# Kernel optimization log

Measured on AMD Instinct MI355X. Metric: run time of the kernel, lower is better.

The kernel has to match this reference:

```python
import jax, jax.numpy as jnp
import numpy as np
from jax import lax

SEQ_LEN = 1024
INPUT_DIM = 64
NUM_HIDDEN = 512
NUM_CLASSES = 10
BATCH = 256
SIGMA = 0.01


def setup_inputs() -> dict:
    key = jax.random.key(0)
    k_x, k_whx, k_whh, k_wph = jax.random.split(key, 4)
    x = jax.random.normal(k_x, (BATCH, SEQ_LEN, INPUT_DIM), dtype=jnp.float32)
    Whx = SIGMA * jax.random.normal(k_whx, (INPUT_DIM, NUM_HIDDEN), dtype=jnp.float32)
    Whh = SIGMA * jax.random.normal(k_whh, (NUM_HIDDEN, NUM_HIDDEN), dtype=jnp.float32)
    Wph = SIGMA * jax.random.normal(k_wph, (NUM_HIDDEN, NUM_CLASSES), dtype=jnp.float32)
    bh = jnp.zeros((NUM_HIDDEN, 1), dtype=jnp.float32)
    bp = jnp.zeros((NUM_CLASSES, 1), dtype=jnp.float32)
    return {"x": x, "Whx": Whx, "Whh": Whh, "Wph": Wph, "bh": bh, "bp": bp}


def reference(x, Whx, Whh, Wph, bh, bp):
    # x: [B, S, D]; h: [B, H]
    B = x.shape[0]
    H = Whh.shape[0]
    bh_row = bh[:, 0]  # per-hidden-unit bias (intended semantics of bh)
    bp_row = bp[:, 0]

    def step(h, xt):
        h_new = jnp.tanh(xt @ Whx + h @ Whh + bh_row)
        return h_new, None

    h0 = jnp.zeros((B, H), dtype=x.dtype)
    xs = jnp.swapaxes(x, 0, 1)  # [S, B, D] for scan over time
    h_final, _ = lax.scan(step, h0, xs)
    p = h_final @ Wph + bp_row  # [B, C]
    return p
```

## Files before the change

### kernel.cpp

```cpp
#include <hip/hip_runtime.h>
#include <hip/hip_bf16.h>
#include <hip/hip_fp8.h>
#include <cstdint>
#include <cstddef>


#define T_SEQ   1024
#define D_IN    64
#define H_DIM   512
#define NB      16
#define NBLK    16
#define NTW     4
#define KS_F16  10
#define KS_REG8 4
#define KS_LDS8 2
#define HSPLIT  320
#define APITCH  848
#define FP8OFF  640
#define ABUF_BYTES (2 * NB * APITCH)
#define WWAVE_BYTES (KS_LDS8 * 2 * 1024)
#define WLDS_BYTES (8 * WWAVE_BYTES)
#define SMEM_TOTAL (ABUF_BYTES + WLDS_BYTES)
#define WSCALE  256.0f
#define HSCALE  128.0f
#define UNSCALE (1.0f / 32768.0f)
#define U_BYTES ((size_t)256 * 1024 * 512 * 2)
#define TT      8
#define NCHUNK  (T_SEQ / TT)
#define NPROD   (NBLK * NCHUNK)
#define FLAG_BYTES (NBLK * NCHUNK * 4)

typedef __attribute__((ext_vector_type(8))) short  short8;
typedef __attribute__((ext_vector_type(4))) short  short4v;
typedef __attribute__((ext_vector_type(4))) float  f32x4;
typedef __attribute__((ext_vector_type(4))) unsigned int uint4v;
typedef __attribute__((ext_vector_type(2))) unsigned int uint2v;

static __device__ __forceinline__ short f16b(float v) {
  return __builtin_bit_cast(short, (_Float16)v);
}
static __device__ __forceinline__ short bf16b(float v) {
  return __builtin_bit_cast(short, __float2bfloat16(v));
}
static __device__ __forceinline__ float f16f(unsigned short u) {
  return (float)__builtin_bit_cast(_Float16, (short)u);
}
static __device__ __forceinline__ unsigned int pk2h(float a, float b) {
#if defined(__has_builtin) && __has_builtin(__builtin_amdgcn_cvt_pkrtz)
  return __builtin_bit_cast(unsigned int, __builtin_amdgcn_cvt_pkrtz(a, b));
#else
  return (unsigned int)(unsigned short)f16b(a) |
         ((unsigned int)(unsigned short)f16b(b) << 16);
#endif
}
static __device__ __forceinline__ float fast_tanh(float x) {
  x = fminf(20.f, fmaxf(-20.f, x));
  const float t = __builtin_amdgcn_exp2f(x * 2.885390081777927f);
  return (t - 1.f) * __builtin_amdgcn_rcpf(t + 1.f);
}
static __device__ __forceinline__ unsigned char f32_to_fp8(float v) {
#if defined(__has_builtin) && __has_builtin(__builtin_amdgcn_cvt_pk_fp8_f32)
  const int r = __builtin_amdgcn_cvt_pk_fp8_f32(v, v, 0, false);
  return (unsigned char)(r & 0xff);
#else
  __hip_fp8_e4m3 f(v);
  return (unsigned char)f.__x;
#endif
}
static __device__ __forceinline__ unsigned int pk4fp8(float a, float b, float c, float d) {
#if defined(__has_builtin) && __has_builtin(__builtin_amdgcn_cvt_pk_fp8_f32)
  int r = __builtin_amdgcn_cvt_pk_fp8_f32(a, b, 0, false);
  r = __builtin_amdgcn_cvt_pk_fp8_f32(c, d, r, true);
  return (unsigned int)r;
#else
  return (unsigned int)f32_to_fp8(a) | ((unsigned int)f32_to_fp8(b) << 8) |
         ((unsigned int)f32_to_fp8(c) << 16) | ((unsigned int)f32_to_fp8(d) << 24);
#endif
}
static __device__ __forceinline__ float fp8_to_f32(unsigned char b) {
  __hip_fp8_e4m3 f;
  f.__x = (__hip_fp8_storage_t)b;
  return (float)f;
}

static __device__ __forceinline__ void producer_body(
    int pid, const float* __restrict__ x, const float* __restrict__ Whx,
    const float* __restrict__ bh, char* __restrict__ U,
    unsigned int* __restrict__ flags)
{
  const int wg = pid & (NBLK - 1);
  const int tc = pid >> 4;
  const int tid  = threadIdx.x;
  const int lane = tid & 63;
  const int w    = tid >> 6;
  const int n16  = lane & 15;
  const int kq   = lane >> 4;
  const int rbase = wg * NB;
  const int cwave = w * 64;

  short8 wa[2][NTW];
  #pragma unroll
  for (int s = 0; s < 2; ++s) {
    #pragma unroll
    for (int nt = 0; nt < NTW; ++nt) {
      const int c = cwave + nt * 16 + n16;
      short8 f;
      #pragma unroll
      for (int j = 0; j < 8; ++j)
        f[j] = f16b(Whx[(size_t)(s * 32 + kq * 8 + j) * H_DIM + c]);
      wa[s][nt] = f;
    }
  }
  f32x4 bb[NTW];
  #pragma unroll
  for (int nt = 0; nt < NTW; ++nt) {
    #pragma unroll
    for (int i = 0; i < 4; ++i) bb[nt][i] = bh[cwave + nt * 16 + kq * 4 + i];
  }

  const int b = rbase + n16;
  for (int tt = 0; tt < TT; ++tt) {
    const int t = tc * TT + tt;
    short8 xb[2];
    #pragma unroll
    for (int s = 0; s < 2; ++s) {
      const float* px = x + ((size_t)b * T_SEQ + t) * D_IN + s * 32 + kq * 8;
      const f32x4 v0 = *(const f32x4*)px;
      const f32x4 v1 = *(const f32x4*)(px + 4);
      short8 f;
      f[0]=f16b(v0.x); f[1]=f16b(v0.y); f[2]=f16b(v0.z); f[3]=f16b(v0.w);
      f[4]=f16b(v1.x); f[5]=f16b(v1.y); f[6]=f16b(v1.z); f[7]=f16b(v1.w);
      xb[s] = f;
    }
    f32x4 D[NTW];
    #pragma unroll
    for (int nt = 0; nt < NTW; ++nt) {
      D[nt] = bb[nt];
      D[nt] = __builtin_amdgcn_mfma_f32_16x16x32_f16(wa[0][nt], xb[0], D[nt], 0, 0, 0);
      D[nt] = __builtin_amdgcn_mfma_f32_16x16x32_f16(wa[1][nt], xb[1], D[nt], 0, 0, 0);
    }
    uint4v o0, o1;
    o0.x = pk2h(D[0][0], D[0][1]); o0.y = pk2h(D[0][2], D[0][3]);
    o0.z = pk2h(D[1][0], D[1][1]); o0.w = pk2h(D[1][2], D[1][3]);
    o1.x = pk2h(D[2][0], D[2][1]); o1.y = pk2h(D[2][2], D[2][3]);
    o1.z = pk2h(D[3][0], D[3][1]); o1.w = pk2h(D[3][2], D[3][3]);
    char* dst = U + (((size_t)t * NBLK + wg) * 512 + tid) * 32;
    *(uint4v*)dst = o0;
    *(uint4v*)(dst + 16) = o1;
  }

  __syncthreads();
  if (flags && tid == 0) {
    __threadfence();
    atomicExch(&flags[wg * NCHUNK + tc], 1u);
  }
}

static __device__ __forceinline__ void consumer_body(
    int wg, const float* __restrict__ Whh, const float* __restrict__ Wph,
    const float* __restrict__ bp, const char* __restrict__ U,
    unsigned int* __restrict__ flags, int gated, float* __restrict__ out)
{
  const int tid  = threadIdx.x;
  const int lane = tid & 63;
  const int w    = tid >> 6;
  const int n16  = lane & 15;
  const int kq   = lane >> 4;
  const int rbase = wg * NB;
  const int cwave = w * 64;

  extern __shared__ char smem[];
  char* Ab  = smem;
  char* Wlw = smem + ABUF_BYTES + w * WWAVE_BYTES;

  short8 wr[KS_F16][NTW];
  #pragma unroll
  for (int s = 0; s < KS_F16; ++s) {
    #pragma unroll
    for (int nt = 0; nt < NTW; ++nt) {
      const int c = cwave + nt * 16 + n16;
      short8 f;
      #pragma unroll
      for (int j = 0; j < 8; ++j)
        f[j] = f16b(Whh[(size_t)(s * 32 + kq * 8 + j) * H_DIM + c]);
      wr[s][nt] = f;
    }
  }
  long long wf8[KS_REG8][NTW];
  #pragma unroll
  for (int s = 0; s < KS_REG8; ++s) {
    #pragma unroll
    for (int nt = 0; nt < NTW; ++nt) {
      const int c  = cwave + nt * 16 + n16;
      const int k0 = (KS_F16 + s) * 32 + kq * 8;
      unsigned int lo = 0, hi = 0;
      #pragma unroll
      for (int bi = 0; bi < 4; ++bi) {
        lo |= ((unsigned int)f32_to_fp8(Whh[(size_t)(k0 + bi) * H_DIM + c] * WSCALE)) << (8 * bi);
        hi |= ((unsigned int)f32_to_fp8(Whh[(size_t)(k0 + 4 + bi) * H_DIM + c] * WSCALE)) << (8 * bi);
      }
      wf8[s][nt] = (long long)(((unsigned long long)hi << 32) | lo);
    }
  }
  for (int sl = 0; sl < KS_LDS8; ++sl) {
    for (int half = 0; half < 2; ++half) {
      const int k0 = (KS_F16 + KS_REG8 + sl) * 32 + kq * 8;
      unsigned int bqq[4];
      #pragma unroll
      for (int hh = 0; hh < 2; ++hh) {
        const int c = cwave + (2 * half + hh) * 16 + n16;
        #pragma unroll
        for (int u = 0; u < 2; ++u) {
          unsigned int acc = 0;
          #pragma unroll
          for (int bi = 0; bi < 4; ++bi)
            acc |= ((unsigned int)f32_to_fp8(Whh[(size_t)(k0 + u * 4 + bi) * H_DIM + c] * WSCALE)) << (8 * bi);
          bqq[hh * 2 + u] = acc;
        }
      }
      uint4v pk; pk.x = bqq[0]; pk.y = bqq[1]; pk.z = bqq[2]; pk.w = bqq[3];
      *(uint4v*)(Wlw + (size_t)(sl * 2 + half) * 1024 + lane * 16) = pk;
    }
  }

  for (int i = tid; i < ABUF_BYTES / 4; i += 512) ((int*)Ab)[i] = 0;
  if (gated) {
    if (tid == 0) {
      while (atomicAdd(&flags[wg * NCHUNK + 0], 0u) == 0u) { }
      __threadfence();
    }
  }
  __syncthreads();
  uint4v Upf0, Upf1;
  {
    const char* up = U + (((size_t)0 * NBLK + wg) * 512 + tid) * 32;
    Upf0 = *(const uint4v*)up;
    Upf1 = *(const uint4v*)(up + 16);
  }

  f32x4 C[NTW], C2[NTW];

  for (int t = 0; t < T_SEQ; ++t) {
    __syncthreads();
    char* Ac = Ab + (t & 1) * (NB * APITCH);
    char* An = Ab + ((t + 1) & 1) * (NB * APITCH);

    short8 hb = *(const short8*)(Ac + n16 * APITCH + 0 * 64 + kq * 16);

    C[0][0]=f16f(Upf0.x&0xffff); C[0][1]=f16f(Upf0.x>>16);
    C[0][2]=f16f(Upf0.y&0xffff); C[0][3]=f16f(Upf0.y>>16);
    C[1][0]=f16f(Upf0.z&0xffff); C[1][1]=f16f(Upf0.z>>16);
    C[1][2]=f16f(Upf0.w&0xffff); C[1][3]=f16f(Upf0.w>>16);
    C[2][0]=f16f(Upf1.x&0xffff); C[2][1]=f16f(Upf1.x>>16);
    C[2][2]=f16f(Upf1.y&0xffff); C[2][3]=f16f(Upf1.y>>16);
    C[3][0]=f16f(Upf1.z&0xffff); C[3][1]=f16f(Upf1.z>>16);
    C[3][2]=f16f(Upf1.w&0xffff); C[3][3]=f16f(Upf1.w>>16);
    #pragma unroll
    for (int nt = 0; nt < NTW; ++nt) C2[nt] = (f32x4){0.f, 0.f, 0.f, 0.f};

    {
      const int t1 = (t + 1 < T_SEQ) ? (t + 1) : (T_SEQ - 1);
      const char* up = U + (((size_t)t1 * NBLK + wg) * 512 + tid) * 32;
      Upf0 = *(const uint4v*)up;
      Upf1 = *(const uint4v*)(up + 16);
    }

    #pragma unroll
    for (int s = 0; s < KS_F16; ++s) {
      const short8 a = hb;
      if (s + 1 < KS_F16)
        hb = *(const short8*)(Ac + n16 * APITCH + (s + 1) * 64 + kq * 16);
      #pragma unroll
      for (int nt = 0; nt < NTW; ++nt)
        C[nt] = __builtin_amdgcn_mfma_f32_16x16x32_f16(wr[s][nt], a, C[nt], 0, 0, 0);
    }

    #pragma unroll
    for (int s = 0; s < KS_REG8; ++s) {
      const long long h8 = *(const long long*)(Ac + n16 * APITCH + FP8OFF + s * 32 + kq * 8);
      #pragma unroll
      for (int nt = 0; nt < NTW; ++nt)
        C2[nt] = __builtin_amdgcn_mfma_f32_16x16x32_fp8_fp8(wf8[s][nt], h8, C2[nt], 0, 0, 0);
    }
    #pragma unroll
    for (int sl = 0; sl < KS_LDS8; ++sl) {
      const long long h8 = *(const long long*)(Ac + n16 * APITCH + FP8OFF + (KS_REG8 + sl) * 32 + kq * 8);
      const uint4v q0 = *(const uint4v*)(Wlw + (size_t)(sl * 2 + 0) * 1024 + lane * 16);
      const uint4v q1 = *(const uint4v*)(Wlw + (size_t)(sl * 2 + 1) * 1024 + lane * 16);
      const long long w0 = (long long)(((unsigned long long)q0.y << 32) | q0.x);
      const long long w1 = (long long)(((unsigned long long)q0.w << 32) | q0.z);
      const long long w2 = (long long)(((unsigned long long)q1.y << 32) | q1.x);
      const long long w3 = (long long)(((unsigned long long)q1.w << 32) | q1.z);
      C2[0] = __builtin_amdgcn_mfma_f32_16x16x32_fp8_fp8(w0, h8, C2[0], 0, 0, 0);
      C2[1] = __builtin_amdgcn_mfma_f32_16x16x32_fp8_fp8(w1, h8, C2[1], 0, 0, 0);
      C2[2] = __builtin_amdgcn_mfma_f32_16x16x32_fp8_fp8(w2, h8, C2[2], 0, 0, 0);
      C2[3] = __builtin_amdgcn_mfma_f32_16x16x32_fp8_fp8(w3, h8, C2[3], 0, 0, 0);
    }

    char* drow = An + n16 * APITCH;
    if (cwave < HSPLIT) {
      #pragma unroll
      for (int nt = 0; nt < NTW; ++nt) {
        const int c0 = cwave + nt * 16 + kq * 4;
        float v0 = fast_tanh(fmaf(C2[nt][0], UNSCALE, C[nt][0]));
        float v1 = fast_tanh(fmaf(C2[nt][1], UNSCALE, C[nt][1]));
        float v2 = fast_tanh(fmaf(C2[nt][2], UNSCALE, C[nt][2]));
        float v3 = fast_tanh(fmaf(C2[nt][3], UNSCALE, C[nt][3]));
        uint2v o; o.x = pk2h(v0, v1); o.y = pk2h(v2, v3);
        *(uint2v*)(drow + c0 * 2) = o;
      }
    } else {
      #pragma unroll
      for (int nt = 0; nt < NTW; ++nt) {
        const int c0 = cwave + nt * 16 + kq * 4;
        float v0 = fast_tanh(fmaf(C2[nt][0], UNSCALE, C[nt][0]));
        float v1 = fast_tanh(fmaf(C2[nt][1], UNSCALE, C[nt][1]));
        float v2 = fast_tanh(fmaf(C2[nt][2], UNSCALE, C[nt][2]));
        float v3 = fast_tanh(fmaf(C2[nt][3], UNSCALE, C[nt][3]));
        *(unsigned int*)(drow + FP8OFF + (c0 - HSPLIT)) =
            pk4fp8(v0 * HSCALE, v1 * HSCALE, v2 * HSCALE, v3 * HSCALE);
      }
    }

    if (gated) {
      const int tn = t + 2;
      if (tn < T_SEQ && (tn & (TT - 1)) == 0) {
        if (tid == 0) {
          while (atomicAdd(&flags[wg * NCHUNK + (tn >> 3)], 0u) == 0u) { }
          __threadfence();
        }
      }
    }
  }

  __syncthreads();
  if (tid < NB * 10) {
    const int r = tid / 10, c = tid % 10;
    const char* row = Ab + r * APITCH;
    float acc = bp[c];
    #pragma unroll 8
    for (int k = 0; k < HSPLIT; ++k)
      acc += f16f(*(const unsigned short*)(row + k * 2)) * Wph[k * 10 + c];
    #pragma unroll 8
    for (int k = HSPLIT; k < H_DIM; ++k)
      acc += fp8_to_f32((unsigned char)row[FP8OFF + (k - HSPLIT)]) * (1.f / HSCALE) * Wph[k * 10 + c];
    out[(size_t)(rbase + r) * 10 + c] = acc;
  }
}

__global__ __launch_bounds__(512, 2)
void VanillaRNN_70025146794452_kernel(
    const float* __restrict__ x, const float* __restrict__ Whx,
    const float* __restrict__ Whh, const float* __restrict__ Wph,
    const float* __restrict__ bh, const float* __restrict__ bp,
    char* __restrict__ U, unsigned int* __restrict__ flags,
    float* __restrict__ out, int mode)
{
  if (mode == 0) {
    if (blockIdx.x < NBLK)
      consumer_body(blockIdx.x, Whh, Wph, bp, U, flags, 1, out);
    else
      producer_body(blockIdx.x - NBLK, x, Whx, bh, U, flags);
  } else if (mode == 1) {
    producer_body(blockIdx.x, x, Whx, bh, U, nullptr);
  } else {
    consumer_body(blockIdx.x, Whh, Wph, bp, U, nullptr, 0, out);
  }
}

#define FB_APITCH  1040
#define FB_FP8OFF  768
#define FB_ABUF    (2 * NB * FB_APITCH)
#define FB_WWAVE   (6 * 2 * 1024)
#define FB_SMEM    (FB_ABUF + 8 * FB_WWAVE)

__global__ __launch_bounds__(512, 2)
void rnn_fallback_kernel(
    const float* __restrict__ x, const float* __restrict__ Whx,
    const float* __restrict__ Whh, const float* __restrict__ Wph,
    const float* __restrict__ bh, const float* __restrict__ bp,
    float* __restrict__ out)
{
  const int tid = threadIdx.x, lane = tid & 63, w = tid >> 6;
  const int n16 = lane & 15, kq = lane >> 4;
  const int rbase = blockIdx.x * NB, cwave = w * 64;
  extern __shared__ char smem[];
  char* Ab  = smem;
  char* Wlw = smem + FB_ABUF + w * FB_WWAVE;

  short8 wr[12 * 4];
  #pragma unroll
  for (int s = 0; s < 12; ++s)
    #pragma unroll
    for (int nt = 0; nt < 4; ++nt) {
      const int c = cwave + nt * 16 + n16, k0 = s * 32 + kq * 8;
      short8 f;
      #pragma unroll
      for (int j = 0; j < 8; ++j) {
        const int k = k0 + j;
        const float* src = (k < D_IN) ? (Whx + (size_t)k * H_DIM + c)
                                      : (Whh + (size_t)(k - D_IN) * H_DIM + c);
        f[j] = bf16b(*src);
      }
      wr[s * 4 + nt] = f;
    }
  for (int s = 0; s < 6; ++s)
    for (int pp = 0; pp < 2; ++pp) {
      const int k0 = (12 + s) * 32 + kq * 8;
      unsigned int bq[4];
      #pragma unroll
      for (int half = 0; half < 2; ++half) {
        const int c = cwave + (2 * pp + half) * 16 + n16;
        #pragma unroll
        for (int u = 0; u < 2; ++u) {
          unsigned int acc = 0;
          #pragma unroll
          for (int bi = 0; bi < 4; ++bi)
            acc |= ((unsigned int)f32_to_fp8(Whh[(size_t)(k0 + u * 4 + bi - D_IN) * H_DIM + c] * WSCALE)) << (8 * bi);
          bq[half * 2 + u] = acc;
        }
      }
      uint4v pk; pk.x = bq[0]; pk.y = bq[1]; pk.z = bq[2]; pk.w = bq[3];
      *(uint4v*)(Wlw + (size_t)(s * 2 + pp) * 1024 + lane * 16) = pk;
    }
  float bhreg[4];
  #pragma unroll
  for (int nt = 0; nt < 4; ++nt) bhreg[nt] = bh[cwave + nt * 16 + n16];
  for (int i = tid; i < FB_ABUF / 4; i += 512) ((int*)Ab)[i] = 0;
  const int xr = (tid >> 4) & 15, xc4 = (tid & 15) * 4;
  if (tid < 256) {
    const f32x4 xv = *(const f32x4*)(x + ((size_t)(rbase + xr) * T_SEQ) * D_IN + xc4);
    short4v s4; s4[0]=bf16b(xv.x); s4[1]=bf16b(xv.y); s4[2]=bf16b(xv.z); s4[3]=bf16b(xv.w);
    *(short4v*)(Ab + xr * FB_APITCH + xc4 * 2) = s4;
  }
  f32x4 C[4], C2[4];
  for (int t = 0; t < T_SEQ; ++t) {
    __syncthreads();
    char* Ac = Ab + (t & 1) * (NB * FB_APITCH);
    char* An = Ab + ((t + 1) & 1) * (NB * FB_APITCH);
    const int t1 = (t + 1 < T_SEQ) ? (t + 1) : (T_SEQ - 1);
    f32x4 xv;
    if (tid < 256)
      xv = *(const f32x4*)(x + ((size_t)(rbase + xr) * T_SEQ + t1) * D_IN + xc4);
    #pragma unroll
    for (int nt = 0; nt < 4; ++nt) {
      C[nt] = (f32x4){0.f,0.f,0.f,0.f}; C2[nt] = (f32x4){0.f,0.f,0.f,0.f};
    }
    #pragma unroll
    for (int s = 0; s < 12; ++s) {
      const short8 a = *(const short8*)(Ac + n16 * FB_APITCH + s * 64 + kq * 16);
      #pragma unroll
      for (int nt = 0; nt < 4; ++nt)
        C[nt] = __builtin_amdgcn_mfma_f32_16x16x32_bf16(a, wr[s * 4 + nt], C[nt], 0, 0, 0);
    }
    #pragma unroll
    for (int s = 0; s < 6; ++s) {
      const long long a8 = *(const long long*)(Ac + n16 * FB_APITCH + FB_FP8OFF + s * 32 + kq * 8);
      #pragma unroll
      for (int pp = 0; pp < 2; ++pp) {
        const uint4v q = *(const uint4v*)(Wlw + (size_t)(s * 2 + pp) * 1024 + lane * 16);
        const long long b0 = (long long)(((unsigned long long)q.y << 32) | q.x);
        const long long b1 = (long long)(((unsigned long long)q.w << 32) | q.z);
        C2[2*pp]   = __builtin_amdgcn_mfma_f32_16x16x32_fp8_fp8(a8, b0, C2[2*pp],   0, 0, 0);
        C2[2*pp+1] = __builtin_amdgcn_mfma_f32_16x16x32_fp8_fp8(a8, b1, C2[2*pp+1], 0, 0, 0);
      }
    }
    if (tid < 256) {
      short4v s4; s4[0]=bf16b(xv.x); s4[1]=bf16b(xv.y); s4[2]=bf16b(xv.z); s4[3]=bf16b(xv.w);
      *(short4v*)(An + xr * FB_APITCH + xc4 * 2) = s4;
    }
    const int row0 = kq * 4;
    #pragma unroll
    for (int nt = 0; nt < 4; ++nt) {
      const int cbase = cwave + nt * 16;
      #pragma unroll
      for (int i = 0; i < 4; ++i) {
        const float v = fast_tanh(fmaf(C2[nt][i], UNSCALE, C[nt][i]) + bhreg[nt]);
        char* dst = An + (row0 + i) * FB_APITCH;
        if (cbase < 320) *(short*)(dst + 128 + (cbase + n16) * 2) = bf16b(v);
        else dst[FB_FP8OFF + (cbase + n16 - 320)] = f32_to_fp8(v * HSCALE);
      }
    }
  }
  __syncthreads();
  if (tid < NB * 10) {
    const int r = tid / 10, c = tid % 10;
    const char* row = Ab + r * FB_APITCH;
    float acc = bp[c];
    #pragma unroll 8
    for (int k = 0; k < 320; ++k) {
      const __hip_bfloat16 hb = __builtin_bit_cast(__hip_bfloat16, *(const short*)(row + 128 + k * 2));
      acc += __bfloat162float(hb) * Wph[k * 10 + c];
    }
    #pragma unroll 8
    for (int k = 320; k < H_DIM; ++k)
      acc += fp8_to_f32((unsigned char)row[FB_FP8OFF + (k - 320)]) * (1.f / HSCALE) * Wph[k * 10 + c];
    out[(size_t)(rbase + r) * 10 + c] = acc;
  }
}

extern "C" void kernel_launch(void* const* d_in, const int* in_sizes, int n_in,
                              void* d_out, int out_size, void* d_ws, size_t ws_size,
                              hipStream_t stream) {
  const float* x   = (const float*)d_in[0];
  const float* Whx = (const float*)d_in[1];
  const float* Whh = (const float*)d_in[2];
  const float* Wph = (const float*)d_in[3];
  const float* bh  = (const float*)d_in[4];
  const float* bp  = (const float*)d_in[5];
  float* out = (float*)d_out;

  if (ws_size >= U_BYTES + FLAG_BYTES + 256) {
    char* U = (char*)d_ws;
    const size_t foff = (ws_size - FLAG_BYTES) & ~(size_t)255;
    unsigned int* flags = (unsigned int*)((char*)d_ws + foff);
    (void)hipFuncSetAttribute((const void*)VanillaRNN_70025146794452_kernel,
                              hipFuncAttributeMaxDynamicSharedMemorySize, SMEM_TOTAL);
    (void)hipMemsetAsync(flags, 0, FLAG_BYTES, stream);
    VanillaRNN_70025146794452_kernel<<<dim3(NBLK + NPROD), dim3(512), SMEM_TOTAL, stream>>>(
        x, Whx, Whh, Wph, bh, bp, U, flags, out, 0);
  } else if (ws_size >= U_BYTES) {
    char* U = (char*)d_ws;
    (void)hipFuncSetAttribute((const void*)VanillaRNN_70025146794452_kernel,
                              hipFuncAttributeMaxDynamicSharedMemorySize, SMEM_TOTAL);
    VanillaRNN_70025146794452_kernel<<<dim3(NPROD), dim3(512), SMEM_TOTAL, stream>>>(
        x, Whx, Whh, Wph, bh, bp, U, nullptr, out, 1);
    VanillaRNN_70025146794452_kernel<<<dim3(NBLK), dim3(512), SMEM_TOTAL, stream>>>(
        x, Whx, Whh, Wph, bh, bp, U, nullptr, out, 2);
  } else {
    (void)hipFuncSetAttribute((const void*)rnn_fallback_kernel,
                              hipFuncAttributeMaxDynamicSharedMemorySize, FB_SMEM);
    rnn_fallback_kernel<<<dim3(NBLK), dim3(512), FB_SMEM, stream>>>(
        x, Whx, Whh, Wph, bh, bp, out);
  }
}
```

Measured before the change: 2.011 ms.

## Compute first timesteps' input projection in consumers to avoid waiting on producers

Consumer blocks now compute the input projection themselves for the first T0 steps, so the recurrence starts without waiting for the first producer chunk. Producers only cover steps T0 onward. The per-chunk gate moves to a per-wave spin before each prefetch instead of a single-thread wait. The split of Whh fp8 slices between registers and LDS shifts toward LDS, launch bounds drop to one block per CU, and the two-kernel non-gated path is removed. The extra Whx registers and the changed weight split could raise register pressure or add LDS traffic on the serial critical path.

```diff
diff --git a/kernel.cpp b/kernel.cpp
--- a/kernel.cpp
+++ b/kernel.cpp
@@ -12,8 +12,8 @@
 #define NBLK    16
 #define NTW     4
 #define KS_F16  10
-#define KS_REG8 4
-#define KS_LDS8 2
+#define KS_REG8 2
+#define KS_LDS8 4
 #define HSPLIT  320
 #define APITCH  848
 #define FP8OFF  640
@@ -24,11 +24,13 @@
 #define WSCALE  256.0f
 #define HSCALE  128.0f
 #define UNSCALE (1.0f / 32768.0f)
-#define U_BYTES ((size_t)256 * 1024 * 512 * 2)
+#define T0      8
 #define TT      8
-#define NCHUNK  (T_SEQ / TT)
+#define NCHUNK  ((T_SEQ - T0) / TT)
 #define NPROD   (NBLK * NCHUNK)
-#define FLAG_BYTES (NBLK * NCHUNK * 4)
+#define UOFF    8192
+#define U2_BYTES ((size_t)(T_SEQ - T0) * NBLK * 512 * 32)
+#define WS_NEED  (UOFF + U2_BYTES)
 
 typedef __attribute__((ext_vector_type(8))) short  short8;
 typedef __attribute__((ext_vector_type(4))) short  short4v;
@@ -81,6 +83,14 @@
   __hip_fp8_e4m3 f;
   f.__x = (__hip_fp8_storage_t)b;
   return (float)f;
+}
+
+static __device__ __forceinline__ void wave_gate(volatile unsigned int* f,
+                                                 unsigned int* fa) {
+  if ((threadIdx.x & 63) == 0) {
+    while (atomicAdd(fa, 0u) == 0u) { }
+  }
+  __threadfence();
 }
 
 static __device__ __forceinline__ void producer_body(
@@ -95,7 +105,6 @@
   const int w    = tid >> 6;
   const int n16  = lane & 15;
   const int kq   = lane >> 4;
-  const int rbase = wg * NB;
   const int cwave = w * 64;
 
   short8 wa[2][NTW];
@@ -118,9 +127,9 @@
     for (int i = 0; i < 4; ++i) bb[nt][i] = bh[cwave + nt * 16 + kq * 4 + i];
   }
 
-  const int b = rbase + n16;
+  const int b = wg * NB + n16;
   for (int tt = 0; tt < TT; ++tt) {
-    const int t = tc * TT + tt;
+    const int t = T0 + tc * TT + tt;
     short8 xb[2];
     #pragma unroll
     for (int s = 0; s < 2; ++s) {
@@ -144,22 +153,24 @@
     o0.z = pk2h(D[1][0], D[1][1]); o0.w = pk2h(D[1][2], D[1][3]);
     o1.x = pk2h(D[2][0], D[2][1]); o1.y = pk2h(D[2][2], D[2][3]);
     o1.z = pk2h(D[3][0], D[3][1]); o1.w = pk2h(D[3][2], D[3][3]);
-    char* dst = U + (((size_t)t * NBLK + wg) * 512 + tid) * 32;
+    char* dst = U + (((size_t)(t - T0) * NBLK + wg) * 512 + tid) * 32;
     *(uint4v*)dst = o0;
     *(uint4v*)(dst + 16) = o1;
   }
 
   __syncthreads();
-  if (flags && tid == 0) {
+  if (threadIdx.x == 0) {
     __threadfence();
-    atomicExch(&flags[wg * NCHUNK + tc], 1u);
+    atomicExch(&flags[wg * 128 + tc], 1u);
   }
 }
 
 static __device__ __forceinline__ void consumer_body(
-    int wg, const float* __restrict__ Whh, const float* __restrict__ Wph,
-    const float* __restrict__ bp, const char* __restrict__ U,
-    unsigned int* __restrict__ flags, int gated, float* __restrict__ out)
+    int wg, const float* __restrict__ x, const float* __restrict__ Whx,
+    const float* __restrict__ Whh, const float* __restrict__ Wph,
+    const float* __restrict__ bh, const float* __restrict__ bp,
+    const char* __restrict__ U, unsigned int* __restrict__ flags, int gated,
+    float* __restrict__ out)
 {
   const int tid  = threadIdx.x;
   const int lane = tid & 63;
@@ -222,47 +233,54 @@
       *(uint4v*)(Wlw + (size_t)(sl * 2 + half) * 1024 + lane * 16) = pk;
     }
   }
+  short8 wa[2][NTW];
+  #pragma unroll
+  for (int s = 0; s < 2; ++s) {
+    #pragma unroll
+    for (int nt = 0; nt < NTW; ++nt) {
+      const int c = cwave + nt * 16 + n16;
+      short8 f;
+      #pragma unroll
+      for (int j = 0; j < 8; ++j)
+        f[j] = f16b(Whx[(size_t)(s * 32 + kq * 8 + j) * H_DIM + c]);
+      wa[s][nt] = f;
+    }
+  }
+  f32x4 bb[NTW];
+  #pragma unroll
+  for (int nt = 0; nt < NTW; ++nt) {
+    #pragma unroll
+    for (int i = 0; i < 4; ++i) bb[nt][i] = bh[cwave + nt * 16 + kq * 4 + i];
+  }
 
   for (int i = tid; i < ABUF_BYTES / 4; i += 512) ((int*)Ab)[i] = 0;
-  if (gated) {
-    if (tid == 0) {
-      while (atomicAdd(&flags[wg * NCHUNK + 0], 0u) == 0u) { }
-      __threadfence();
-    }
-  }
-  __syncthreads();
-  uint4v Upf0, Upf1;
-  {
-    const char* up = U + (((size_t)0 * NBLK + wg) * 512 + tid) * 32;
-    Upf0 = *(const uint4v*)up;
-    Upf1 = *(const uint4v*)(up + 16);
-  }
 
   f32x4 C[NTW], C2[NTW];
 
-  for (int t = 0; t < T_SEQ; ++t) {
+  for (int t = 0; t < T0; ++t) {
     __syncthreads();
     char* Ac = Ab + (t & 1) * (NB * APITCH);
     char* An = Ab + ((t + 1) & 1) * (NB * APITCH);
 
     short8 hb = *(const short8*)(Ac + n16 * APITCH + 0 * 64 + kq * 16);
 
-    C[0][0]=f16f(Upf0.x&0xffff); C[0][1]=f16f(Upf0.x>>16);
-    C[0][2]=f16f(Upf0.y&0xffff); C[0][3]=f16f(Upf0.y>>16);
-    C[1][0]=f16f(Upf0.z&0xffff); C[1][1]=f16f(Upf0.z>>16);
-    C[1][2]=f16f(Upf0.w&0xffff); C[1][3]=f16f(Upf0.w>>16);
-    C[2][0]=f16f(Upf1.x&0xffff); C[2][1]=f16f(Upf1.x>>16);
-    C[2][2]=f16f(Upf1.y&0xffff); C[2][3]=f16f(Upf1.y>>16);
-    C[3][0]=f16f(Upf1.z&0xffff); C[3][1]=f16f(Upf1.z>>16);
-    C[3][2]=f16f(Upf1.w&0xffff); C[3][3]=f16f(Upf1.w>>16);
-    #pragma unroll
-    for (int nt = 0; nt < NTW; ++nt) C2[nt] = (f32x4){0.f, 0.f, 0.f, 0.f};
-
-    {
-      const int t1 = (t + 1 < T_SEQ) ? (t + 1) : (T_SEQ - 1);
-      const char* up = U + (((size_t)t1 * NBLK + wg) * 512 + tid) * 32;
-      Upf0 = *(const uint4v*)up;
-      Upf1 = *(const uint4v*)(up + 16);
+    short8 xb[2];
+    #pragma unroll
+    for (int s = 0; s < 2; ++s) {
+      const float* px = x + ((size_t)(rbase + n16) * T_SEQ + t) * D_IN + s * 32 + kq * 8;
+      const f32x4 v0 = *(const f32x4*)px;
+      const f32x4 v1 = *(const f32x4*)(px + 4);
+      short8 f;
+      f[0]=f16b(v0.x); f[1]=f16b(v0.y); f[2]=f16b(v0.z); f[3]=f16b(v0.w);
+      f[4]=f16b(v1.x); f[5]=f16b(v1.y); f[6]=f16b(v1.z); f[7]=f16b(v1.w);
+      xb[s] = f;
+    }
+    #pragma unroll
+    for (int nt = 0; nt < NTW; ++nt) {
+      C[nt] = bb[nt];
+      C[nt] = __builtin_amdgcn_mfma_f32_16x16x32_f16(wa[0][nt], xb[0], C[nt], 0, 0, 0);
+      C[nt] = __builtin_amdgcn_mfma_f32_16x16x32_f16(wa[1][nt], xb[1], C[nt], 0, 0, 0);
+      C2[nt] = (f32x4){0.f, 0.f, 0.f, 0.f};
     }
 
     #pragma unroll
@@ -274,7 +292,6 @@
       for (int nt = 0; nt < NTW; ++nt)
         C[nt] = __builtin_amdgcn_mfma_f32_16x16x32_f16(wr[s][nt], a, C[nt], 0, 0, 0);
     }
-
     #pragma unroll
     for (int s = 0; s < KS_REG8; ++s) {
       const long long h8 = *(const long long*)(Ac + n16 * APITCH + FP8OFF + s * 32 + kq * 8);
@@ -321,14 +338,98 @@
             pk4fp8(v0 * HSCALE, v1 * HSCALE, v2 * HSCALE, v3 * HSCALE);
       }
     }
-
-    if (gated) {
-      const int tn = t + 2;
-      if (tn < T_SEQ && (tn & (TT - 1)) == 0) {
-        if (tid == 0) {
-          while (atomicAdd(&flags[wg * NCHUNK + (tn >> 3)], 0u) == 0u) { }
-          __threadfence();
-        }
+  }
+
+  if (gated) wave_gate(&flags[wg * 128 + 0], &flags[wg * 128 + 0]);
+  uint4v Upf0, Upf1;
+  {
+    const char* up = U + (((size_t)0 * NBLK + wg) * 512 + tid) * 32;
+    Upf0 = *(const uint4v*)up;
+    Upf1 = *(const uint4v*)(up + 16);
+  }
+
+  for (int t = T0; t < T_SEQ; ++t) {
+    __syncthreads();
+    char* Ac = Ab + (t & 1) * (NB * APITCH);
+    char* An = Ab + ((t + 1) & 1) * (NB * APITCH);
+
+    short8 hb = *(const short8*)(Ac + n16 * APITCH + 0 * 64 + kq * 16);
+
+    C[0][0]=f16f(Upf0.x&0xffff); C[0][1]=f16f(Upf0.x>>16);
+    C[0][2]=f16f(Upf0.y&0xffff); C[0][3]=f16f(Upf0.y>>16);
+    C[1][0]=f16f(Upf0.z&0xffff); C[1][1]=f16f(Upf0.z>>16);
+    C[1][2]=f16f(Upf0.w&0xffff); C[1][3]=f16f(Upf0.w>>16);
+    C[2][0]=f16f(Upf1.x&0xffff); C[2][1]=f16f(Upf1.x>>16);
+    C[2][2]=f16f(Upf1.y&0xffff); C[2][3]=f16f(Upf1.y>>16);
+    C[3][0]=f16f(Upf1.z&0xffff); C[3][1]=f16f(Upf1.z>>16);
+    C[3][2]=f16f(Upf1.w&0xffff); C[3][3]=f16f(Upf1.w>>16);
+    #pragma unroll
+    for (int nt = 0; nt < NTW; ++nt) C2[nt] = (f32x4){0.f, 0.f, 0.f, 0.f};
+
+    {
+      const int t1 = (t + 1 < T_SEQ) ? (t + 1) : (T_SEQ - 1);
+      if (gated && (t1 & (TT - 1)) == 0 && t1 > T0) {
+        const int c1 = (t1 - T0) >> 3;
+        wave_gate(&flags[wg * 128 + c1], &flags[wg * 128 + c1]);
+      }
+      const char* up = U + (((size_t)(t1 - T0) * NBLK + wg) * 512 + tid) * 32;
+      Upf0 = *(const uint4v*)up;
+      Upf1 = *(const uint4v*)(up + 16);
+    }
+
+    #pragma unroll
+    for (int s = 0; s < KS_F16; ++s) {
+      const short8 a = hb;
+      if (s + 1 < KS_F16)
+        hb = *(const short8*)(Ac + n16 * APITCH + (s + 1) * 64 + kq * 16);
+      #pragma unroll
+      for (int nt = 0; nt < NTW; ++nt)
+        C[nt] = __builtin_amdgcn_mfma_f32_16x16x32_f16(wr[s][nt], a, C[nt], 0, 0, 0);
+    }
+    #pragma unroll
+    for (int s = 0; s < KS_REG8; ++s) {
+      const long long h8 = *(const long long*)(Ac + n16 * APITCH + FP8OFF + s * 32 + kq * 8);
+      #pragma unroll
+      for (int nt = 0; nt < NTW; ++nt)
+        C2[nt] = __builtin_amdgcn_mfma_f32_16x16x32_fp8_fp8(wf8[s][nt], h8, C2[nt], 0, 0, 0);
+    }
+    #pragma unroll
+    for (int sl = 0; sl < KS_LDS8; ++sl) {
+      const long long h8 = *(const long long*)(Ac + n16 * APITCH + FP8OFF + (KS_REG8 + sl) * 32 + kq * 8);
+      const uint4v q0 = *(const uint4v*)(Wlw + (size_t)(sl * 2 + 0) * 1024 + lane * 16);
+      const uint4v q1 = *(const uint4v*)(Wlw + (size_t)(sl * 2 + 1) * 1024 + lane * 16);
+      const long long w0 = (long long)(((unsigned long long)q0.y << 32) | q0.x);
+      const long long w1 = (long long)(((unsigned long long)q0.w << 32) | q0.z);
+      const long long w2 = (long long)(((unsigned long long)q1.y << 32) | q1.x);
+      const long long w3 = (long long)(((unsigned long long)q1.w << 32) | q1.z);
+      C2[0] = __builtin_amdgcn_mfma_f32_16x16x32_fp8_fp8(w0, h8, C2[0], 0, 0, 0);
+      C2[1] = __builtin_amdgcn_mfma_f32_16x16x32_fp8_fp8(w1, h8, C2[1], 0, 0, 0);
+      C2[2] = __builtin_amdgcn_mfma_f32_16x16x32_fp8_fp8(w2, h8, C2[2], 0, 0, 0);
+      C2[3] = __builtin_amdgcn_mfma_f32_16x16x32_fp8_fp8(w3, h8, C2[3], 0, 0, 0);
+    }
+
+    char* drow = An + n16 * APITCH;
+    if (cwave < HSPLIT) {
+      #pragma unroll
+      for (int nt = 0; nt < NTW; ++nt) {
+        const int c0 = cwave + nt * 16 + kq * 4;
+        float v0 = fast_tanh(fmaf(C2[nt][0], UNSCALE, C[nt][0]));
+        float v1 = fast_tanh(fmaf(C2[nt][1], UNSCALE, C[nt][1]));
+        float v2 = fast_tanh(fmaf(C2[nt][2], UNSCALE, C[nt][2]));
+        float v3 = fast_tanh(fmaf(C2[nt][3], UNSCALE, C[nt][3]));
+        uint2v o; o.x = pk2h(v0, v1); o.y = pk2h(v2, v3);
+        *(uint2v*)(drow + c0 * 2) = o;
+      }
+    } else {
+      #pragma unroll
+      for (int nt = 0; nt < NTW; ++nt) {
+        const int c0 = cwave + nt * 16 + kq * 4;
+        float v0 = fast_tanh(fmaf(C2[nt][0], UNSCALE, C[nt][0]));
+        float v1 = fast_tanh(fmaf(C2[nt][1], UNSCALE, C[nt][1]));
+        float v2 = fast_tanh(fmaf(C2[nt][2], UNSCALE, C[nt][2]));
+        float v3 = fast_tanh(fmaf(C2[nt][3], UNSCALE, C[nt][3]));
+        *(unsigned int*)(drow + FP8OFF + (c0 - HSPLIT)) =
+            pk4fp8(v0 * HSCALE, v1 * HSCALE, v2 * HSCALE, v3 * HSCALE);
       }
     }
   }
@@ -348,24 +449,18 @@
   }
 }
 
-__global__ __launch_bounds__(512, 2)
+__global__ __launch_bounds__(512, 1)
 void VanillaRNN_70025146794452_kernel(
     const float* __restrict__ x, const float* __restrict__ Whx,
     const float* __restrict__ Whh, const float* __restrict__ Wph,
     const float* __restrict__ bh, const float* __restrict__ bp,
     char* __restrict__ U, unsigned int* __restrict__ flags,
-    float* __restrict__ out, int mode)
+    float* __restrict__ out)
 {
-  if (mode == 0) {
-    if (blockIdx.x < NBLK)
-      consumer_body(blockIdx.x, Whh, Wph, bp, U, flags, 1, out);
-    else
-      producer_body(blockIdx.x - NBLK, x, Whx, bh, U, flags);
-  } else if (mode == 1) {
-    producer_body(blockIdx.x, x, Whx, bh, U, nullptr);
-  } else {
-    consumer_body(blockIdx.x, Whh, Wph, bp, U, nullptr, 0, out);
-  }
+  if (blockIdx.x < NBLK)
+    consumer_body(blockIdx.x, x, Whx, Whh, Wph, bh, bp, U, flags, 1, out);
+  else
+    producer_body(blockIdx.x - NBLK, x, Whx, bh, U, flags);
 }
 
 #define FB_APITCH  1040
@@ -510,23 +605,14 @@
   const float* bp  = (const float*)d_in[5];
   float* out = (float*)d_out;
 
-  if (ws_size >= U_BYTES + FLAG_BYTES + 256) {
-    char* U = (char*)d_ws;
-    const size_t foff = (ws_size - FLAG_BYTES) & ~(size_t)255;
-    unsigned int* flags = (unsigned int*)((char*)d_ws + foff);
+  if (ws_size >= WS_NEED) {
+    unsigned int* flags = (unsigned int*)d_ws;
+    char* U = (char*)d_ws + UOFF;
     (void)hipFuncSetAttribute((const void*)VanillaRNN_70025146794452_kernel,
                               hipFuncAttributeMaxDynamicSharedMemorySize, SMEM_TOTAL);
-    (void)hipMemsetAsync(flags, 0, FLAG_BYTES, stream);
+    (void)hipMemsetAsync(flags, 0, UOFF, stream);
     VanillaRNN_70025146794452_kernel<<<dim3(NBLK + NPROD), dim3(512), SMEM_TOTAL, stream>>>(
-        x, Whx, Whh, Wph, bh, bp, U, flags, out, 0);
-  } else if (ws_size >= U_BYTES) {
-    char* U = (char*)d_ws;
-    (void)hipFuncSetAttribute((const void*)VanillaRNN_70025146794452_kernel,
-                              hipFuncAttributeMaxDynamicSharedMemorySize, SMEM_TOTAL);
-    VanillaRNN_70025146794452_kernel<<<dim3(NPROD), dim3(512), SMEM_TOTAL, stream>>>(
-        x, Whx, Whh, Wph, bh, bp, U, nullptr, out, 1);
-    VanillaRNN_70025146794452_kernel<<<dim3(NBLK), dim3(512), SMEM_TOTAL, stream>>>(
-        x, Whx, Whh, Wph, bh, bp, U, nullptr, out, 2);
+        x, Whx, Whh, Wph, bh, bp, U, flags, out);
   } else {
     (void)hipFuncSetAttribute((const void*)rnn_fallback_kernel,
                               hipFuncAttributeMaxDynamicSharedMemorySize, FB_SMEM);
```

Measured after the change: 2.747 ms. 1.37x slower.
